# Optimization experiments

Measured on AMD Instinct MI355X. Metric: run time of the kernel, lower is better.

## Reference

```python
import jax, jax.numpy as jnp
import numpy as np

HIDDEN = 256

def setup_inputs() -> dict:
    key = jax.random.key(0)
    ks = jax.random.split(key, 8)
    B, N1, N2, D = 4, 4096, 4096, 256
    s = 1.0 / np.sqrt(D)
    return {
        "inputs1": jax.random.normal(ks[0], (B, N1, D), jnp.float32),
        "inputs2": jax.random.normal(ks[1], (B, N2, D), jnp.float32),
        "mask": jax.random.randint(ks[2], (B, N1, N2), 0, 2, jnp.int32),
        "Wq": jax.random.normal(ks[3], (D, HIDDEN), jnp.float32) * s,
        "bq": jnp.zeros((HIDDEN,), jnp.float32),
        "Wk": jax.random.normal(ks[4], (D, HIDDEN), jnp.float32) * s,
        "bk": jnp.zeros((HIDDEN,), jnp.float32),
        "Wv": jax.random.normal(ks[5], (D, HIDDEN), jnp.float32) * s,
        "bv": jnp.zeros((HIDDEN,), jnp.float32),
    }

def reference(inputs1, inputs2, mask, Wq, bq, Wk, bk, Wv, bv):
    # q: (B,N1,H), k,v: (B,N2,H)
    q = inputs1 @ Wq + bq
    k = inputs2 @ Wk + bk
    v = inputs2 @ Wv + bv
    scale = 1.0 / np.sqrt(HIDDEN)
    # scores: (B,N1,N2)
    scores = jnp.einsum('bnh,bmh->bnm', q, k) * scale
    # original: masked_fill(mask <= 0, 1e-9) -- NOT -inf; replicate faithfully
    scores = jnp.where(mask <= 0, jnp.float32(1e-9), scores)
    attn = jax.nn.softmax(scores, axis=-1)
    return jnp.einsum('bnm,bmh->bnh', attn, v)
```

## Files before the change

kernel.cpp:

```cpp
#include <hip/hip_runtime.h>

typedef float  f32x4 __attribute__((ext_vector_type(4)));
typedef short  s16x8 __attribute__((ext_vector_type(8)));
typedef short  s16x4 __attribute__((ext_vector_type(4)));

#define MFMA16(a,b,c) __builtin_amdgcn_mfma_f32_16x16x32_bf16(a,b,c,0,0,0)

static __device__ __forceinline__ f32x4 mfma_pv(s16x4 a, s16x4 b, f32x4 c){
#if defined(__HIP_DEVICE_COMPILE__)
    return __builtin_amdgcn_mfma_f32_16x16x16bf16_1k(a, b, c, 0, 0, 0);
#else
    (void)a; (void)b; return c;
#endif
}

static __device__ __forceinline__ unsigned short f2bf(float f){
    union { float f; unsigned int u; } x; x.f = f;
    unsigned int r = x.u + 0x7fffu + ((x.u >> 16) & 1u);
    return (unsigned short)(r >> 16);
}

__global__ void wt_prep(const float* __restrict__ Wq, const float* __restrict__ Wk,
                        const float* __restrict__ Wv, unsigned short* __restrict__ wt){
    const int p = blockIdx.y;
    const int o8 = blockIdx.x*256 + threadIdx.x;
    const float* W = (p==0) ? Wq : ((p==1) ? Wk : Wv);
    const int lane = o8 & 63, t = (o8 >> 6) & 15, ks = o8 >> 10;
    const int quad = lane >> 4, lq = lane & 15;
    s16x8 o;
    #pragma unroll
    for(int j=0;j<8;j++)
        o[j] = (short)f2bf(W[(ks*32 + quad*8 + j)*256 + 16*t + lq]);
    *(s16x8*)(wt + (size_t)p*65536 + (size_t)o8*8) = o;
}

static __device__ __forceinline__ void stage_x(const float* x, size_t row0,
                                               int tid, unsigned short* sX){
    const float* xg = x + row0*256;
    #pragma unroll
    for(int rr=0; rr<16; rr++){
        int c = tid + rr*256;
        int row = c>>6, cc = c&63;
        float4 f = *(const float4*)(xg + row*256 + cc*4);
        unsigned short* d = &sX[row*264 + cc*4];
        d[0]=f2bf(f.x); d[1]=f2bf(f.y); d[2]=f2bf(f.z); d[3]=f2bf(f.w);
    }
}

__global__ __launch_bounds__(256) void proj_all(const float* __restrict__ x1,
        const float* __restrict__ x2, const unsigned short* __restrict__ wt,
        const float* __restrict__ bq, const float* __restrict__ bk,
        const float* __restrict__ bv, int b0,
        unsigned short* __restrict__ qdst, unsigned short* __restrict__ kfrag,
        unsigned short* __restrict__ vfrag){
    const int rt = blockIdx.x, p = blockIdx.y, z = blockIdx.z;
    const int zz = b0 + z;
    const int tid = threadIdx.x, w = tid>>6, lane = tid&63, quad = lane>>4, lq = lane&15;
    __shared__ __align__(16) unsigned short sX[64*264];

    const float* x = (p==0) ? x1 : x2;
    stage_x(x, (size_t)(zz*64 + rt)*64, tid, sX);
    __syncthreads();

    s16x8 a[8];
    #pragma unroll
    for(int ks=0; ks<8; ks++)
        a[ks] = *(const s16x8*)(&sX[(16*w+lq)*264 + ks*32 + quad*8]);

    f32x4 acc[16];
    #pragma unroll
    for(int t=0;t<16;t++) acc[t] = (f32x4)(0.0f);
    const unsigned short* wtp = wt + (size_t)p*65536;
    #pragma unroll
    for(int ks=0; ks<8; ks++){
        #pragma unroll
        for(int t=0; t<16; t++){
            s16x8 bf_ = *(const s16x8*)(wtp + (((size_t)(ks*16 + t)*64 + lane)*8));
            acc[t] = MFMA16(a[ks], bf_, acc[t]);
        }
    }

    if(p == 0){
        #pragma unroll
        for(int t=0;t<16;t++){
            float bvf = bq[16*t+lq];
            #pragma unroll
            for(int r=0;r<4;r++){
                size_t row = (size_t)(zz*64 + rt)*64 + 16*w + 4*quad + r;
                qdst[row*256 + 16*t + lq] = f2bf(acc[t][r] + bvf);
            }
        }
    } else if(p == 1){
        __syncthreads();
        #pragma unroll
        for(int t=0;t<16;t++){
            float bvf = bk[16*t+lq];
            #pragma unroll
            for(int r=0;r<4;r++)
                sX[(16*w + 4*quad + r)*264 + 16*t + lq] = f2bf(acc[t][r] + bvf);
        }
        __syncthreads();
        unsigned short* kd = kfrag + (size_t)z*1048576;
        #pragma unroll
        for(int ks=0; ks<8; ks++){
            s16x8 v = *(const s16x8*)(&sX[(16*w + lq)*264 + 32*ks + 8*quad]);
            *(s16x8*)(kd + ((((size_t)rt*4 + w)*8 + ks)*64 + lane)*8) = v;
        }
    } else {
        unsigned short* vd = vfrag + (size_t)z*1048576;
        #pragma unroll
        for(int t2=0; t2<8; t2++){
            float b0f = bv[16*(2*t2  )+lq];
            float b1f = bv[16*(2*t2+1)+lq];
            s16x8 o;
            #pragma unroll
            for(int r=0;r<4;r++){
                o[r]   = (short)f2bf(acc[2*t2  ][r] + b0f);
                o[4+r] = (short)f2bf(acc[2*t2+1][r] + b1f);
            }
            *(s16x8*)(vd + ((((size_t)rt*4 + w)*8 + t2)*64 + lane)*8) = o;
        }
    }
}

__global__ __launch_bounds__(512,2) void attn(
        const unsigned short* __restrict__ qb, const unsigned short* __restrict__ kfrag,
        const unsigned short* __restrict__ vfrag, const int* __restrict__ mask,
        float* __restrict__ out, int b0){
    const int bid = blockIdx.x;
    int b, qt, bk_;
    if(gridDim.x == 512){ b = (bid&7)>>1; qt = (bid>>3)*2 + (bid&1); bk_ = b; }
    else                { b = b0; qt = bid; bk_ = 0; }
    const int tid = threadIdx.x, w4 = tid>>6, lane = tid&63, quad = lane>>4, lq = lane&15;
    const int half = w4>>2, w = w4&3;
    const int qbase = qt*32;
    const int kt0 = half*32;

    __shared__ __align__(16) unsigned char smem[67648];

    s16x8 qf[2][8];
    #pragma unroll
    for(int rg=0; rg<2; rg++){
        size_t row = (size_t)(b*4096 + qbase + 16*rg + lq);
        #pragma unroll
        for(int ks=0; ks<8; ks++)
            qf[rg][ks] = *(const s16x8*)(qb + row*256 + ks*32 + quad*8);
    }

    f32x4 oacc[16][2];
    #pragma unroll
    for(int t=0;t<16;t++){ oacc[t][0] = (f32x4)(0.0f); oacc[t][1] = (f32x4)(0.0f); }
    float rsum[2] = {0.0f, 0.0f};

    const unsigned char* kfb = (const unsigned char*)(kfrag + (size_t)bk_*1048576);
    const unsigned char* vfb = (const unsigned char*)(vfrag + (size_t)bk_*1048576);
    const int* mp0 = mask + ((size_t)(b*4096 + qbase) + lq)*4096 + 16*w + 4*quad;

    int4 mA0 = *(const int4*)(mp0 + (size_t)kt0*64);
    int4 mA1 = *(const int4*)(mp0 + (size_t)16*4096 + kt0*64);

    for(int kt=kt0; kt<kt0+32; kt++){
        const unsigned char* gK = kfb + (size_t)kt*32768;
        const unsigned char* gV = vfb + (size_t)kt*32768;

        f32x4 sacc0 = (f32x4)(0.0f), sacc1 = (f32x4)(0.0f);
        {
            s16x8 kf_[4];
            #pragma unroll
            for(int ks=0; ks<4; ks++)
                kf_[ks] = *(const s16x8*)(gK + (((unsigned)(w*8 + ks)*64 + lane)*16));
            #pragma unroll
            for(int ks=0; ks<4; ks++){
                sacc0 = MFMA16(kf_[ks], qf[0][ks], sacc0);
                sacc1 = MFMA16(kf_[ks], qf[1][ks], sacc1);
            }
            #pragma unroll
            for(int ks=0; ks<4; ks++)
                kf_[ks] = *(const s16x8*)(gK + (((unsigned)(w*8 + 4 + ks)*64 + lane)*16));
            #pragma unroll
            for(int ks=0; ks<4; ks++){
                sacc0 = MFMA16(kf_[ks], qf[0][4+ks], sacc0);
                sacc1 = MFMA16(kf_[ks], qf[1][4+ks], sacc1);
            }
        }

        s16x4 pb0, pb1;
        {
            float p;
            p = (mA0.x>0)?__expf(sacc0[0]*0.0625f):1.0f; rsum[0]+=p; pb0[0]=(short)f2bf(p);
            p = (mA0.y>0)?__expf(sacc0[1]*0.0625f):1.0f; rsum[0]+=p; pb0[1]=(short)f2bf(p);
            p = (mA0.z>0)?__expf(sacc0[2]*0.0625f):1.0f; rsum[0]+=p; pb0[2]=(short)f2bf(p);
            p = (mA0.w>0)?__expf(sacc0[3]*0.0625f):1.0f; rsum[0]+=p; pb0[3]=(short)f2bf(p);
            p = (mA1.x>0)?__expf(sacc1[0]*0.0625f):1.0f; rsum[1]+=p; pb1[0]=(short)f2bf(p);
            p = (mA1.y>0)?__expf(sacc1[1]*0.0625f):1.0f; rsum[1]+=p; pb1[1]=(short)f2bf(p);
            p = (mA1.z>0)?__expf(sacc1[2]*0.0625f):1.0f; rsum[1]+=p; pb1[2]=(short)f2bf(p);
            p = (mA1.w>0)?__expf(sacc1[3]*0.0625f):1.0f; rsum[1]+=p; pb1[3]=(short)f2bf(p);
        }

        if(kt < 63){
            mA0 = *(const int4*)(mp0 + (size_t)(kt+1)*64);
            mA1 = *(const int4*)(mp0 + (size_t)16*4096 + (kt+1)*64);
        }

        {
            s16x8 vf_[4];
            #pragma unroll
            for(int t2=0; t2<4; t2++)
                vf_[t2] = *(const s16x8*)(gV + (((unsigned)(w*8 + t2)*64 + lane)*16));
            #pragma unroll
            for(int t2=0; t2<4; t2++){
                s16x4 vlo = __builtin_shufflevector(vf_[t2], vf_[t2], 0,1,2,3);
                s16x4 vhi = __builtin_shufflevector(vf_[t2], vf_[t2], 4,5,6,7);
                oacc[2*t2  ][0] = mfma_pv(vlo, pb0, oacc[2*t2  ][0]);
                oacc[2*t2  ][1] = mfma_pv(vlo, pb1, oacc[2*t2  ][1]);
                oacc[2*t2+1][0] = mfma_pv(vhi, pb0, oacc[2*t2+1][0]);
                oacc[2*t2+1][1] = mfma_pv(vhi, pb1, oacc[2*t2+1][1]);
            }
            #pragma unroll
            for(int t2=0; t2<4; t2++)
                vf_[t2] = *(const s16x8*)(gV + (((unsigned)(w*8 + 4 + t2)*64 + lane)*16));
            #pragma unroll
            for(int t2=0; t2<4; t2++){
                s16x4 vlo = __builtin_shufflevector(vf_[t2], vf_[t2], 0,1,2,3);
                s16x4 vhi = __builtin_shufflevector(vf_[t2], vf_[t2], 4,5,6,7);
                oacc[2*(4+t2)  ][0] = mfma_pv(vlo, pb0, oacc[2*(4+t2)  ][0]);
                oacc[2*(4+t2)  ][1] = mfma_pv(vlo, pb1, oacc[2*(4+t2)  ][1]);
                oacc[2*(4+t2)+1][0] = mfma_pv(vhi, pb0, oacc[2*(4+t2)+1][0]);
                oacc[2*(4+t2)+1][1] = mfma_pv(vhi, pb1, oacc[2*(4+t2)+1][1]);
            }
        }
    }

    float* sRS  = (float*)smem;
    float* sRed = (float*)(smem + 1024);
    #pragma unroll
    for(int rg=0; rg<2; rg++){
        float v = rsum[rg];
        v += __shfl_xor(v, 16);
        v += __shfl_xor(v, 32);
        if(quad == 0) sRS[w4*32 + 16*rg + lq] = v;
    }
    for(int c=0; c<4; c++){
        __syncthreads();
        #pragma unroll
        for(int tt=0; tt<4; tt++){
            int t = 4*c + tt;
            #pragma unroll
            for(int rg=0; rg<2; rg++){
                #pragma unroll
                for(int r=0; r<4; r++)
                    sRed[w4*2081 + (16*rg+lq)*65 + 16*tt + 4*quad + r] = oacc[t][rg][r];
            }
        }
        __syncthreads();
        #pragma unroll
        for(int j=0; j<4; j++){
            int idx = j*512 + tid;
            int hl = idx & 63, q = idx >> 6;
            float s  = sRed[0*2081 + q*65+hl] + sRed[1*2081 + q*65+hl]
                     + sRed[2*2081 + q*65+hl] + sRed[3*2081 + q*65+hl]
                     + sRed[4*2081 + q*65+hl] + sRed[5*2081 + q*65+hl]
                     + sRed[6*2081 + q*65+hl] + sRed[7*2081 + q*65+hl];
            float rs = sRS[0*32+q] + sRS[1*32+q] + sRS[2*32+q] + sRS[3*32+q]
                     + sRS[4*32+q] + sRS[5*32+q] + sRS[6*32+q] + sRS[7*32+q];
            out[((size_t)(b*4096 + qbase + q))*256 + 64*c + hl] = s / rs;
        }
    }
}

extern "C" void kernel_launch(void* const* d_in, const int* in_sizes, int n_in,
                              void* d_out, int out_size, void* d_ws, size_t ws_size,
                              hipStream_t stream){
    (void)in_sizes; (void)n_in; (void)out_size;
    const float* x1 = (const float*)d_in[0];
    const float* x2 = (const float*)d_in[1];
    const int*   mk = (const int*)  d_in[2];
    const float* Wq = (const float*)d_in[3];
    const float* bq = (const float*)d_in[4];
    const float* Wk = (const float*)d_in[5];
    const float* bk = (const float*)d_in[6];
    const float* Wv = (const float*)d_in[7];
    const float* bv = (const float*)d_in[8];
    float* out = (float*)d_out;
    char* ws = (char*)d_ws;

    unsigned short* wt = (unsigned short*)ws;
    unsigned short* qb = (unsigned short*)(ws + 393216);
    const size_t kvoff = 393216 + 8388608;

    wt_prep<<<dim3(32,3), 256, 0, stream>>>(Wq, Wk, Wv, wt);

    if(ws_size >= kvoff + 16ull*1024*1024){
        unsigned short* kf = (unsigned short*)(ws + kvoff);
        unsigned short* vf = (unsigned short*)(ws + kvoff + 8388608);
        proj_all<<<dim3(64,3,4), 256, 0, stream>>>(x1, x2, wt, bq, bk, bv, 0,
                                                   qb, kf, vf);
        attn<<<512, 512, 0, stream>>>(qb, kf, vf, mk, out, 0);
    } else {
        unsigned short* kf = (unsigned short*)(ws + kvoff);
        unsigned short* vf = (unsigned short*)(ws + kvoff + 2097152);
        for(int b=0;b<4;b++){
            proj_all<<<dim3(64,3,1), 256, 0, stream>>>(x1, x2, wt, bq, bk, bv, b,
                                                       qb, kf, vf);
            attn<<<128, 512, 0, stream>>>(qb, kf, vf, mk, out, b);
        }
    }
}
```

Before: 552.6 us.

## Pack int32 mask into bitmask during projection, read bits in attention

Measured after the change: 683.7 us. 1.24x slower.

```diff
diff --git a/kernel.cpp b/kernel.cpp
--- a/kernel.cpp
+++ b/kernel.cpp
@@ -3,6 +3,7 @@
 typedef float  f32x4 __attribute__((ext_vector_type(4)));
 typedef short  s16x8 __attribute__((ext_vector_type(8)));
 typedef short  s16x4 __attribute__((ext_vector_type(4)));
+typedef int    i32x4 __attribute__((ext_vector_type(4)));
 
 #define MFMA16(a,b,c) __builtin_amdgcn_mfma_f32_16x16x32_bf16(a,b,c,0,0,0)
 
@@ -52,12 +53,44 @@
         const float* __restrict__ bq, const float* __restrict__ bk,
         const float* __restrict__ bv, int b0,
         unsigned short* __restrict__ qdst, unsigned short* __restrict__ kfrag,
-        unsigned short* __restrict__ vfrag){
+        unsigned short* __restrict__ vfrag,
+        const int* __restrict__ mask, unsigned long long* __restrict__ pm){
     const int rt = blockIdx.x, p = blockIdx.y, z = blockIdx.z;
     const int zz = b0 + z;
     const int tid = threadIdx.x, w = tid>>6, lane = tid&63, quad = lane>>4, lq = lane&15;
+
+    if(p == 3){
+        #pragma unroll 1
+        for(int rr=0; rr<16; rr++){
+            const size_t lrow = (size_t)rt*64 + w*16 + rr;
+            const int* mrow = mask + ((size_t)zz*4096 + lrow)*4096;
+            unsigned long long* prow = pm +
+                ((gridDim.z==4) ? ((size_t)zz*4096 + lrow) : lrow)*64;
+            #pragma unroll 1
+            for(int g=0; g<16; g++){
+                const i32x4* pv = (const i32x4*)(mrow + g*256 + lane*4);
+#if __has_builtin(__builtin_nontemporal_load)
+                i32x4 v = __builtin_nontemporal_load(pv);
+#else
+                i32x4 v = *pv;
+#endif
+                unsigned long long b0_ = __ballot(v.x > 0);
+                unsigned long long b1_ = __ballot(v.y > 0);
+                unsigned long long b2_ = __ballot(v.z > 0);
+                unsigned long long b3_ = __ballot(v.w > 0);
+                if(lane < 4){
+                    unsigned long long wd =  ((b0_>>(16*lane))&0xFFFFull)
+                        | (((b1_>>(16*lane))&0xFFFFull)<<16)
+                        | (((b2_>>(16*lane))&0xFFFFull)<<32)
+                        | (((b3_>>(16*lane))&0xFFFFull)<<48);
+                    prow[g*4 + lane] = wd;
+                }
+            }
+        }
+        return;
+    }
+
     __shared__ __align__(16) unsigned short sX[64*264];
-
     const float* x = (p==0) ? x1 : x2;
     stage_x(x, (size_t)(zz*64 + rt)*64, tid, sX);
     __syncthreads();
@@ -125,7 +158,8 @@
 
 __global__ __launch_bounds__(512,2) void attn(
         const unsigned short* __restrict__ qb, const unsigned short* __restrict__ kfrag,
-        const unsigned short* __restrict__ vfrag, const int* __restrict__ mask,
+        const unsigned short* __restrict__ vfrag,
+        const unsigned long long* __restrict__ pmask,
         float* __restrict__ out, int b0){
     const int bid = blockIdx.x;
     int b, qt, bk_;
@@ -135,6 +169,7 @@
     const int half = w4>>2, w = w4&3;
     const int qbase = qt*32;
     const int kt0 = half*32;
+    const size_t rowb = (gridDim.x == 512) ? (size_t)b*4096 : 0;
 
     __shared__ __align__(16) unsigned char smem[67648];
 
@@ -154,10 +189,12 @@
 
     const unsigned char* kfb = (const unsigned char*)(kfrag + (size_t)bk_*1048576);
     const unsigned char* vfb = (const unsigned char*)(vfrag + (size_t)bk_*1048576);
-    const int* mp0 = mask + ((size_t)(b*4096 + qbase) + lq)*4096 + 16*w + 4*quad;
-
-    int4 mA0 = *(const int4*)(mp0 + (size_t)kt0*64);
-    int4 mA1 = *(const int4*)(mp0 + (size_t)16*4096 + kt0*64);
+    const unsigned long long* pm0 = pmask + ((size_t)(rowb + qbase) + lq)*64;
+    const unsigned long long* pm1 = pm0 + 16*64;
+    const int sh = 4*w + quad;
+
+    unsigned long long mM0 = pm0[kt0] >> sh;
+    unsigned long long mM1 = pm1[kt0] >> sh;
 
     for(int kt=kt0; kt<kt0+32; kt++){
         const unsigned char* gK = kfb + (size_t)kt*32768;
@@ -187,19 +224,19 @@
         s16x4 pb0, pb1;
         {
             float p;
-            p = (mA0.x>0)?__expf(sacc0[0]*0.0625f):1.0f; rsum[0]+=p; pb0[0]=(short)f2bf(p);
-            p = (mA0.y>0)?__expf(sacc0[1]*0.0625f):1.0f; rsum[0]+=p; pb0[1]=(short)f2bf(p);
-            p = (mA0.z>0)?__expf(sacc0[2]*0.0625f):1.0f; rsum[0]+=p; pb0[2]=(short)f2bf(p);
-            p = (mA0.w>0)?__expf(sacc0[3]*0.0625f):1.0f; rsum[0]+=p; pb0[3]=(short)f2bf(p);
-            p = (mA1.x>0)?__expf(sacc1[0]*0.0625f):1.0f; rsum[1]+=p; pb1[0]=(short)f2bf(p);
-            p = (mA1.y>0)?__expf(sacc1[1]*0.0625f):1.0f; rsum[1]+=p; pb1[1]=(short)f2bf(p);
-            p = (mA1.z>0)?__expf(sacc1[2]*0.0625f):1.0f; rsum[1]+=p; pb1[2]=(short)f2bf(p);
-            p = (mA1.w>0)?__expf(sacc1[3]*0.0625f):1.0f; rsum[1]+=p; pb1[3]=(short)f2bf(p);
+            p = (mM0     &1)? __expf(sacc0[0]*0.0625f):1.0f; rsum[0]+=p; pb0[0]=(short)f2bf(p);
+            p = ((mM0>>16)&1)? __expf(sacc0[1]*0.0625f):1.0f; rsum[0]+=p; pb0[1]=(short)f2bf(p);
+            p = ((mM0>>32)&1)? __expf(sacc0[2]*0.0625f):1.0f; rsum[0]+=p; pb0[2]=(short)f2bf(p);
+            p = ((mM0>>48)&1)? __expf(sacc0[3]*0.0625f):1.0f; rsum[0]+=p; pb0[3]=(short)f2bf(p);
+            p = (mM1     &1)? __expf(sacc1[0]*0.0625f):1.0f; rsum[1]+=p; pb1[0]=(short)f2bf(p);
+            p = ((mM1>>16)&1)? __expf(sacc1[1]*0.0625f):1.0f; rsum[1]+=p; pb1[1]=(short)f2bf(p);
+            p = ((mM1>>32)&1)? __expf(sacc1[2]*0.0625f):1.0f; rsum[1]+=p; pb1[2]=(short)f2bf(p);
+            p = ((mM1>>48)&1)? __expf(sacc1[3]*0.0625f):1.0f; rsum[1]+=p; pb1[3]=(short)f2bf(p);
         }
 
         if(kt < 63){
-            mA0 = *(const int4*)(mp0 + (size_t)(kt+1)*64);
-            mA1 = *(const int4*)(mp0 + (size_t)16*4096 + (kt+1)*64);
+            mM0 = pm0[kt+1] >> sh;
+            mM1 = pm1[kt+1] >> sh;
         }
 
         {
@@ -290,19 +327,21 @@
 
     wt_prep<<<dim3(32,3), 256, 0, stream>>>(Wq, Wk, Wv, wt);
 
-    if(ws_size >= kvoff + 16ull*1024*1024){
+    if(ws_size >= kvoff + 25165824ull){
         unsigned short* kf = (unsigned short*)(ws + kvoff);
         unsigned short* vf = (unsigned short*)(ws + kvoff + 8388608);
-        proj_all<<<dim3(64,3,4), 256, 0, stream>>>(x1, x2, wt, bq, bk, bv, 0,
-                                                   qb, kf, vf);
-        attn<<<512, 512, 0, stream>>>(qb, kf, vf, mk, out, 0);
+        unsigned long long* pmb = (unsigned long long*)(ws + kvoff + 16777216);
+        proj_all<<<dim3(64,4,4), 256, 0, stream>>>(x1, x2, wt, bq, bk, bv, 0,
+                                                   qb, kf, vf, mk, pmb);
+        attn<<<512, 512, 0, stream>>>(qb, kf, vf, pmb, out, 0);
     } else {
         unsigned short* kf = (unsigned short*)(ws + kvoff);
         unsigned short* vf = (unsigned short*)(ws + kvoff + 2097152);
+        unsigned long long* pmb = (unsigned long long*)(ws + kvoff + 4194304);
         for(int b=0;b<4;b++){
-            proj_all<<<dim3(64,3,1), 256, 0, stream>>>(x1, x2, wt, bq, bk, bv, b,
-                                                       qb, kf, vf);
-            attn<<<128, 512, 0, stream>>>(qb, kf, vf, mk, out, b);
-        }
-    }
-}
+            proj_all<<<dim3(64,4,1), 256, 0, stream>>>(x1, x2, wt, bq, bk, bv, b,
+                                                       qb, kf, vf, mk, pmb);
+            attn<<<128, 512, 0, stream>>>(qb, kf, vf, pmb, out, b);
+        }
+    }
+}
```
